# Kernel optimization log

Measured on AMD Instinct MI355X. Metric: run time of the kernel, lower is better.

The kernel has to match this reference:

```python
import jax, jax.numpy as jnp
import numpy as np

B, N, DIM, HEADS = 8, 4096, 512, 8
BASE = 10000.0


def rope_cos_sin(n, dim, base=BASE):
    k_max = dim // 2
    theta = 1.0 / base ** (jnp.arange(k_max, dtype=jnp.float32) / k_max)
    angles = jnp.arange(n, dtype=jnp.float32)[:, None] * theta  # (n, k_max)
    return jnp.cos(angles), jnp.sin(angles)


def apply_rope(x, cos, sin):
    # x: (b, n, dim); complex pairs are interleaved (even=real, odd=imag)
    xr = x[..., 0::2]
    xi = x[..., 1::2]
    out_r = cos * xr - sin * xi
    out_i = sin * xr + cos * xi
    return jnp.stack([out_r, out_i], axis=-1).reshape(x.shape)


def setup_inputs() -> dict:
    key = jax.random.key(0)
    ks = jax.random.split(key, 8)
    s = 0.02
    return {
        'x': jax.random.normal(ks[0], (B, N, DIM), jnp.float32),
        'y': jax.random.normal(ks[1], (B, N, DIM), jnp.float32),
        'Wq': jax.random.normal(ks[2], (DIM, DIM), jnp.float32) * s,
        'bq': jax.random.normal(ks[3], (DIM,), jnp.float32) * s,
        'Wk': jax.random.normal(ks[4], (DIM, DIM), jnp.float32) * s,
        'bk': jax.random.normal(ks[5], (DIM,), jnp.float32) * s,
        'lepe_w': jax.random.normal(ks[6], (DIM, 1, 3), jnp.float32) * s,
        'lepe_b': jax.random.normal(ks[7], (DIM,), jnp.float32) * s,
    }


def reference(x, y, Wq, bq, Wk, bk, lepe_w, lepe_b):
    b, n, c = x.shape
    h = HEADS
    d = c // h
    q = jax.nn.elu(x @ Wq.T + bq) + 1.0
    k = jax.nn.elu(y @ Wk.T + bk) + 1.0
    cos, sin = rope_cos_sin(n, c)
    q_rope = apply_rope(q, cos, sin).reshape(b, n, h, d).transpose(0, 2, 1, 3)
    k_rope = apply_rope(k, cos, sin).reshape(b, n, h, d).transpose(0, 2, 1, 3)
    qh = q.reshape(b, n, h, d).transpose(0, 2, 1, 3)
    kh = k.reshape(b, n, h, d).transpose(0, 2, 1, 3)
    v = y.reshape(b, n, h, d).transpose(0, 2, 1, 3)
    kmean = kh.mean(axis=2, keepdims=True)  # (b,h,1,d)
    z = 1.0 / (jnp.einsum('bhnd,bhmd->bhnm', qh, kmean) + 1e-6)  # (b,h,n,1)
    scale = n ** (-0.5)
    kv = jnp.einsum('bhnd,bhne->bhde', k_rope * scale, v * scale)  # (b,h,d,d)
    out = jnp.einsum('bhnd,bhde->bhne', q_rope, kv) * z  # (b,h,n,d)
    out = out.transpose(0, 2, 1, 3).reshape(b, n, c)
    # LePE: depthwise conv1d over value stream
    vc = v.transpose(0, 2, 1, 3).reshape(b, n, c).transpose(0, 2, 1)  # (b,c,n)
    lepe = jax.lax.conv_general_dilated(
        vc, lepe_w, window_strides=(1,), padding=[(1, 1)],
        dimension_numbers=('NCH', 'OIH', 'NCH'), feature_group_count=c)
    lepe = lepe + lepe_b[None, :, None]
    return out + lepe.transpose(0, 2, 1)
```

## Files before the change

kernel.cpp:

```cpp
#include <hip/hip_runtime.h>

#define B_ 8
#define N_ 4096
#define C_ 512
#define H_ 8

typedef _Float16 h8  __attribute__((ext_vector_type(8)));
typedef _Float16 h4v __attribute__((ext_vector_type(4)));
typedef float    f4  __attribute__((ext_vector_type(4)));

static const size_t OFF_COS  = 0;
static const size_t OFF_SIN  = (size_t)4*1024*1024;
static const size_t OFF_KRH  = (size_t)8*1024*1024;
static const size_t OFF_WQH  = (size_t)40*1024*1024;
static const size_t OFF_WKH  = (size_t)40*1024*1024 + 512*1024;
static const size_t OFF_KSUM = (size_t)41*1024*1024;
static const size_t OFF_KVG  = (size_t)41*1024*1024 + 64*1024;
static const size_t OFF_KVT  = (size_t)42*1024*1024 + 64*1024;

__device__ __forceinline__ unsigned int pack2h(float a, float b){
    union { _Float16 h[2]; unsigned int u; } x;
    x.h[0] = (_Float16)a; x.h[1] = (_Float16)b; return x.u;
}

__global__ void k_tables(float* __restrict__ cosT, float* __restrict__ sinT){
    int n = blockIdx.x, j = threadIdx.x;
    double th = exp((double)j * -0.035977892078031970);
    float ang = (float)n * (float)th;
    float s, c; sincosf(ang, &s, &c);
    cosT[n*256 + j] = c; sinT[n*256 + j] = s;
}

__global__ __launch_bounds__(256) void k_prepw(const float* __restrict__ Wq, const float* __restrict__ Wk,
                                               _Float16* __restrict__ Wqh, _Float16* __restrict__ Wkh){
    int u = blockIdx.x*256 + threadIdx.x;
    {
        float4 a = *(const float4*)&Wq[(size_t)u*8];
        float4 b = *(const float4*)&Wq[(size_t)u*8 + 4];
        uint4 o; o.x = pack2h(a.x,a.y); o.y = pack2h(a.z,a.w); o.z = pack2h(b.x,b.y); o.w = pack2h(b.z,b.w);
        *(uint4*)&Wqh[(size_t)u*8] = o;
    }
    {
        float4 a = *(const float4*)&Wk[(size_t)u*8];
        float4 b = *(const float4*)&Wk[(size_t)u*8 + 4];
        uint4 o; o.x = pack2h(a.x,a.y); o.y = pack2h(a.z,a.w); o.z = pack2h(b.x,b.y); o.w = pack2h(b.z,b.w);
        *(uint4*)&Wkh[(size_t)u*8] = o;
    }
}

__device__ __forceinline__ void stage_b(const _Float16* __restrict__ g, _Float16* lds, int t){
#pragma unroll
    for (int i=0;i<2;++i){
        int u = i*256 + t;
        int r = u >> 2;
        int c8 = (u & 3) ^ ((r ^ (r >> 2)) & 3);
        __builtin_amdgcn_global_load_lds(
            (const __attribute__((address_space(1))) void*)(g + (size_t)r*C_ + c8*8),
            (__attribute__((address_space(3))) void*)(lds + (size_t)(i*256 + (t & 192))*8),
            16, 0, 0);
    }
}

template<int IS_Q>
__global__ __launch_bounds__(256, 2) void k_gemm(
    const float* __restrict__ X, const _Float16* __restrict__ Wh, const float* __restrict__ bias,
    const float* __restrict__ cosT, const float* __restrict__ sinT,
    _Float16* __restrict__ krh, float* __restrict__ ksum,
    const float* __restrict__ ksumIn, const _Float16* __restrict__ kvTg,
    const float* __restrict__ y, const float* __restrict__ lw, const float* __restrict__ lb,
    float* __restrict__ outp)
{
    __shared__ __align__(16) char smem[IS_Q ? 55296 : 26624];
    _Float16* As  = (_Float16*)smem;
    _Float16* Bs0 = (_Float16*)(smem + 10240);
    _Float16* Bs1 = (_Float16*)(smem + 18432);
    _Float16* qrs = (_Float16*)smem;
    _Float16* kvs = (_Float16*)(smem + 36864);

    const int t = threadIdx.x;
    const int lane = t & 63;
    const int w = t >> 6;
    const int wm = w >> 1, wn = w & 1;
    const int col0 = blockIdx.x * 128;
    const int row0 = blockIdx.y * 128;
    const int lrow = lane & 15, lg = lane >> 4;
    const int srow = t >> 3;
    const int sc4 = (t & 7) * 4;
    const int b = row0 >> 12;

    if constexpr (IS_Q){
#pragma unroll
        for (int i=0;i<4;++i){
            int idx = i*256 + t;
            int hl = idx >> 9, e = (idx >> 3) & 63, c8 = idx & 7;
            int bhh = b*H_ + (col0 >> 6) + hl;
            *(uint4*)&kvs[hl*4608 + e*72 + c8*8] =
                *(const uint4*)&kvTg[(size_t)bhh*4096 + e*64 + c8*8];
        }
    }

    f4 acc[4][4] = {};
    const float* Xp = X + (size_t)(row0 + srow)*C_ + sc4;
    float4 ra[4];
#pragma unroll
    for (int it=0; it<4; ++it) ra[it] = *(const float4*)(Xp + (size_t)it*32*C_);
    stage_b(Wh + (size_t)col0*C_, Bs0, t);

    const int sw = (lrow ^ (lrow >> 2)) & 3;
    const int cB = (lg ^ sw) * 8;
    _Float16* Bcur = Bs0; _Float16* Bnxt = Bs1;

    for (int kk=0; kk<16; ++kk){
#pragma unroll
        for (int it=0; it<4; ++it){
            int r = srow + it*32;
            h4v a; a[0]=(_Float16)ra[it].x; a[1]=(_Float16)ra[it].y; a[2]=(_Float16)ra[it].z; a[3]=(_Float16)ra[it].w;
            *(h4v*)&As[r*40 + sc4] = a;
        }
        if (kk < 15){
#pragma unroll
            for (int it=0; it<4; ++it)
                ra[it] = *(const float4*)(Xp + (size_t)it*32*C_ + (kk+1)*32);
            stage_b(Wh + (size_t)col0*C_ + (kk+1)*32, Bnxt, t);
        }
        __syncthreads();
        h8 af[4], bf[4];
#pragma unroll
        for (int mi=0; mi<4; ++mi) af[mi] = *(const h8*)&As[(wm*64 + mi*16 + lrow)*40 + lg*8];
#pragma unroll
        for (int ni=0; ni<4; ++ni) bf[ni] = *(const h8*)&Bcur[(wn*64 + ni*16 + lrow)*32 + cB];
#pragma unroll
        for (int mi=0; mi<4; ++mi)
#pragma unroll
            for (int ni=0; ni<4; ++ni)
                acc[mi][ni] = __builtin_amdgcn_mfma_f32_16x16x32_f16(af[mi], bf[ni], acc[mi][ni], 0,0,0);
        __syncthreads();
        _Float16* tmp = Bcur; Bcur = Bnxt; Bnxt = tmp;
    }

    const int hcol0 = col0 + wn*64;
    float bcol[4], km[4];
#pragma unroll
    for (int ni=0; ni<4; ++ni){
        int c = hcol0 + ni*16 + lrow;
        bcol[ni] = bias[c];
        km[ni] = IS_Q ? ksumIn[b*C_ + c] * (1.0f/4096.0f) : 0.0f;
    }
    float colsum[4] = {0.f,0.f,0.f,0.f};
    float zr[4][4];
    _Float16* qw = qrs + w*4608;

#pragma unroll
    for (int mi=0; mi<4; ++mi){
        float qv[4][4];
#pragma unroll
        for (int ni=0; ni<4; ++ni)
#pragma unroll
            for (int r=0; r<4; ++r){
                float v = acc[mi][ni][r] + bcol[ni];
                qv[ni][r] = v > 0.f ? v + 1.f : __expf(v);
            }
        if constexpr (IS_Q){
#pragma unroll
            for (int r=0; r<4; ++r){
                float p = qv[0][r]*km[0] + qv[1][r]*km[1] + qv[2][r]*km[2] + qv[3][r]*km[3];
                p += __shfl_xor(p, 1); p += __shfl_xor(p, 2);
                p += __shfl_xor(p, 4); p += __shfl_xor(p, 8);
                zr[mi][r] = 1.0f / (p + 1e-6f);
            }
        } else {
#pragma unroll
            for (int ni=0; ni<4; ++ni)
                colsum[ni] += qv[ni][0]+qv[ni][1]+qv[ni][2]+qv[ni][3];
        }
#pragma unroll
        for (int ni=0; ni<4; ++ni){
            int c = hcol0 + ni*16 + lrow;
            int jj = c >> 1;
#pragma unroll
            for (int r=0; r<4; ++r){
                int grow = row0 + wm*64 + mi*16 + lg*4 + r;
                int n = grow & (N_-1);
                float val = qv[ni][r];
                float par = __shfl_xor(val, 1);
                float cs = cosT[n*256 + jj], sn = sinT[n*256 + jj];
                float rv = (lane & 1) ? fmaf(sn, par, cs*val) : fmaf(cs, val, -sn*par);
                float prv = __shfl_xor(rv, 1);
                if constexpr (IS_Q){
                    if (!(lane & 1))
                        *(unsigned int*)&qw[(mi*16 + lg*4 + r)*72 + (ni*16 + lrow)] = pack2h(rv, prv);
                } else {
                    if (!(lane & 1))
                        *(unsigned int*)&krh[(size_t)grow*C_ + c] = pack2h(rv, prv);
                }
            }
        }
    }

    if constexpr (!IS_Q){
#pragma unroll
        for (int ni=0; ni<4; ++ni){
            float s = colsum[ni];
            s += __shfl_xor(s, 16); s += __shfl_xor(s, 32);
            if (lane < 16) atomicAdd(&ksum[b*C_ + hcol0 + ni*16 + lane], s);
        }
    } else {
        f4 acc2[4][4] = {};
#pragma unroll
        for (int ks=0; ks<2; ++ks){
            h8 af2[4], bf2[4];
#pragma unroll
            for (int mi2=0; mi2<4; ++mi2) af2[mi2] = *(const h8*)&qw[(mi2*16 + lrow)*72 + ks*32 + lg*8];
#pragma unroll
            for (int ni2=0; ni2<4; ++ni2) bf2[ni2] = *(const h8*)&kvs[wn*4608 + (ni2*16 + lrow)*72 + ks*32 + lg*8];
#pragma unroll
            for (int mi2=0; mi2<4; ++mi2)
#pragma unroll
                for (int ni2=0; ni2<4; ++ni2)
                    acc2[mi2][ni2] = __builtin_amdgcn_mfma_f32_16x16x32_f16(af2[mi2], bf2[ni2], acc2[mi2][ni2], 0,0,0);
        }
        float w0[4], w1[4], w2[4], wb[4];
#pragma unroll
        for (int ni2=0; ni2<4; ++ni2){
            int cc = hcol0 + ni2*16 + lrow;
            w0[ni2]=lw[cc*3+0]; w1[ni2]=lw[cc*3+1]; w2[ni2]=lw[cc*3+2]; wb[ni2]=lb[cc];
        }
#pragma unroll
        for (int mi2=0; mi2<4; ++mi2){
#pragma unroll
            for (int r=0; r<4; ++r){
                int grow = row0 + wm*64 + mi2*16 + lg*4 + r;
                int n = grow & (N_-1);
                float z = zr[mi2][r];
#pragma unroll
                for (int ni2=0; ni2<4; ++ni2){
                    int c = hcol0 + ni2*16 + lrow;
                    const float* yp = y + (size_t)grow*C_ + c;
                    float s = fmaf(yp[0], w1[ni2], wb[ni2]);
                    if (n > 0)      s = fmaf(*(yp - C_), w0[ni2], s);
                    if (n < N_-1)   s = fmaf(*(yp + C_), w2[ni2], s);
                    outp[(size_t)grow*C_ + c] = fmaf(acc2[mi2][ni2][r], z, s);
                }
            }
        }
    }
}

__global__ __launch_bounds__(256) void k_kv(const _Float16* __restrict__ krh, const float* __restrict__ y,
                                            float* __restrict__ kvg){
    __shared__ _Float16 krs[64*128];
    __shared__ _Float16 vs[64*128];
    const int split = blockIdx.x, bh = blockIdx.y;
    const int b = bh >> 3, h = bh & 7;
    const int t = threadIdx.x, lane = t & 63, w = t >> 6;
    const int lrow = lane & 15, lg = lane >> 4;
    f4 acc[4] = {};
    for (int sub=0; sub<4; ++sub){
        const int n0 = split*512 + sub*128;
#pragma unroll
        for (int i=0;i<8;++i){
            int q = i*256 + t;
            int d2 = q & 31, n2 = q >> 5;
            int n = n0 + 2*n2, c = h*64 + 2*d2;
            size_t g0 = (size_t)(b*N_ + n)*C_ + c;
            unsigned int u0 = *(const unsigned int*)&krh[g0];
            unsigned int u1 = *(const unsigned int*)&krh[g0 + C_];
            int chunk = n2 >> 2, j2 = (n2 & 3)*2;
            int pc0 = chunk ^ ((2*d2) & 15);
            int pc1 = pc0 ^ 1;
            *(unsigned int*)&krs[(2*d2)*128 + pc0*8 + j2]   = (u0 & 0xffffu) | (u1 << 16);
            *(unsigned int*)&krs[(2*d2+1)*128 + pc1*8 + j2] = (u0 >> 16) | (u1 & 0xffff0000u);
            float2 a0 = *(const float2*)&y[g0];
            float2 a1 = *(const float2*)&y[g0 + C_];
            *(unsigned int*)&vs[(2*d2)*128 + pc0*8 + j2]   = pack2h(a0.x, a1.x);
            *(unsigned int*)&vs[(2*d2+1)*128 + pc1*8 + j2] = pack2h(a0.y, a1.y);
        }
        __syncthreads();
#pragma unroll
        for (int ks=0; ks<4; ++ks){
            int cu = ((ks*4 + lg) ^ lrow)*8;
            h8 a = *(const h8*)&krs[(w*16 + lrow)*128 + cu];
#pragma unroll
            for (int ni=0; ni<4; ++ni){
                h8 bv = *(const h8*)&vs[(ni*16 + lrow)*128 + cu];
                acc[ni] = __builtin_amdgcn_mfma_f32_16x16x32_f16(a, bv, acc[ni], 0,0,0);
            }
        }
        __syncthreads();
    }
#pragma unroll
    for (int ni=0; ni<4; ++ni)
#pragma unroll
        for (int rr=0; rr<4; ++rr)
            atomicAdd(&kvg[(size_t)bh*4096 + (w*16 + lg*4 + rr)*64 + ni*16 + lrow],
                      acc[ni][rr] * (1.0f/4096.0f));
}

__global__ __launch_bounds__(256) void k_kvmerge(const float* __restrict__ kvg, _Float16* __restrict__ kvTg){
    int bh = blockIdx.x, t = threadIdx.x;
    const float* src = kvg + (size_t)bh*4096;
    _Float16* dst = kvTg + (size_t)bh*4096;
#pragma unroll
    for (int i=0;i<4;++i){
        int q = i*256 + t;
        int e2 = q & 31, d2 = q >> 5;
        float2 a0 = *(const float2*)&src[(2*d2)*64 + 2*e2];
        float2 a1 = *(const float2*)&src[(2*d2+1)*64 + 2*e2];
        *(unsigned int*)&dst[(2*e2)*64 + 2*d2]   = pack2h(a0.x, a1.x);
        *(unsigned int*)&dst[(2*e2+1)*64 + 2*d2] = pack2h(a0.y, a1.y);
    }
}

extern "C" void kernel_launch(void* const* d_in, const int* in_sizes, int n_in,
                              void* d_out, int out_size, void* d_ws, size_t ws_size,
                              hipStream_t stream)
{
    (void)in_sizes; (void)n_in; (void)out_size; (void)ws_size;
    const float* x  = (const float*)d_in[0];
    const float* y  = (const float*)d_in[1];
    const float* Wq = (const float*)d_in[2];
    const float* bq = (const float*)d_in[3];
    const float* Wk = (const float*)d_in[4];
    const float* bk = (const float*)d_in[5];
    const float* lw = (const float*)d_in[6];
    const float* lb = (const float*)d_in[7];

    char* ws = (char*)d_ws;
    float*    cosT = (float*)(ws + OFF_COS);
    float*    sinT = (float*)(ws + OFF_SIN);
    _Float16* krh  = (_Float16*)(ws + OFF_KRH);
    _Float16* Wqh  = (_Float16*)(ws + OFF_WQH);
    _Float16* Wkh  = (_Float16*)(ws + OFF_WKH);
    float*    ksum = (float*)(ws + OFF_KSUM);
    float*    kvg  = (float*)(ws + OFF_KVG);
    _Float16* kvTg = (_Float16*)(ws + OFF_KVT);
    float*    out  = (float*)d_out;

    hipMemsetAsync(ws + OFF_KSUM, 0, 64*1024 + 1024*1024, stream);
    k_tables<<<dim3(N_), dim3(256), 0, stream>>>(cosT, sinT);
    k_prepw<<<dim3(128), dim3(256), 0, stream>>>(Wq, Wk, Wqh, Wkh);
    k_gemm<0><<<dim3(4, 256), dim3(256), 0, stream>>>(y, Wkh, bk, cosT, sinT,
        krh, ksum, nullptr, nullptr, nullptr, nullptr, nullptr, nullptr);
    k_kv<<<dim3(8, 64), dim3(256), 0, stream>>>(krh, y, kvg);
    k_kvmerge<<<dim3(64), dim3(256), 0, stream>>>(kvg, kvTg);
    k_gemm<1><<<dim3(4, 256), dim3(256), 0, stream>>>(x, Wqh, bq, cosT, sinT,
        nullptr, nullptr, ksum, kvTg, y, lw, lb, out);
}
```

Baseline: 199.5 us.

## Double-buffer A tile, raise occupancy, and vectorize LePE epilogue via LDS staging

```diff
diff --git a/kernel.cpp b/kernel.cpp
--- a/kernel.cpp
+++ b/kernel.cpp
@@ -62,7 +62,7 @@
 }
 
 template<int IS_Q>
-__global__ __launch_bounds__(256, 2) void k_gemm(
+__global__ __launch_bounds__(256, IS_Q ? 3 : 4) void k_gemm(
     const float* __restrict__ X, const _Float16* __restrict__ Wh, const float* __restrict__ bias,
     const float* __restrict__ cosT, const float* __restrict__ sinT,
     _Float16* __restrict__ krh, float* __restrict__ ksum,
@@ -70,10 +70,7 @@
     const float* __restrict__ y, const float* __restrict__ lw, const float* __restrict__ lb,
     float* __restrict__ outp)
 {
-    __shared__ __align__(16) char smem[IS_Q ? 55296 : 26624];
-    _Float16* As  = (_Float16*)smem;
-    _Float16* Bs0 = (_Float16*)(smem + 10240);
-    _Float16* Bs1 = (_Float16*)(smem + 18432);
+    __shared__ __align__(16) char smem[IS_Q ? 53248 : 36864];
     _Float16* qrs = (_Float16*)smem;
     _Float16* kvs = (_Float16*)(smem + 36864);
 
@@ -88,57 +85,59 @@
     const int sc4 = (t & 7) * 4;
     const int b = row0 >> 12;
 
-    if constexpr (IS_Q){
-#pragma unroll
-        for (int i=0;i<4;++i){
-            int idx = i*256 + t;
-            int hl = idx >> 9, e = (idx >> 3) & 63, c8 = idx & 7;
-            int bhh = b*H_ + (col0 >> 6) + hl;
-            *(uint4*)&kvs[hl*4608 + e*72 + c8*8] =
-                *(const uint4*)&kvTg[(size_t)bhh*4096 + e*64 + c8*8];
-        }
-    }
-
     f4 acc[4][4] = {};
     const float* Xp = X + (size_t)(row0 + srow)*C_ + sc4;
     float4 ra[4];
 #pragma unroll
     for (int it=0; it<4; ++it) ra[it] = *(const float4*)(Xp + (size_t)it*32*C_);
-    stage_b(Wh + (size_t)col0*C_, Bs0, t);
+    stage_b(Wh + (size_t)col0*C_, (_Float16*)(smem + 20480), t);
 
     const int sw = (lrow ^ (lrow >> 2)) & 3;
     const int cB = (lg ^ sw) * 8;
-    _Float16* Bcur = Bs0; _Float16* Bnxt = Bs1;
+    int cur = 0;
 
     for (int kk=0; kk<16; ++kk){
+        _Float16* As = (_Float16*)(smem + cur*10240);
 #pragma unroll
         for (int it=0; it<4; ++it){
             int r = srow + it*32;
             h4v a; a[0]=(_Float16)ra[it].x; a[1]=(_Float16)ra[it].y; a[2]=(_Float16)ra[it].z; a[3]=(_Float16)ra[it].w;
             *(h4v*)&As[r*40 + sc4] = a;
         }
+        __syncthreads();
         if (kk < 15){
 #pragma unroll
             for (int it=0; it<4; ++it)
                 ra[it] = *(const float4*)(Xp + (size_t)it*32*C_ + (kk+1)*32);
-            stage_b(Wh + (size_t)col0*C_ + (kk+1)*32, Bnxt, t);
-        }
-        __syncthreads();
+            stage_b(Wh + (size_t)col0*C_ + (kk+1)*32, (_Float16*)(smem + 20480 + (cur^1)*8192), t);
+        }
+        _Float16* Bs = (_Float16*)(smem + 20480 + cur*8192);
         h8 af[4], bf[4];
 #pragma unroll
         for (int mi=0; mi<4; ++mi) af[mi] = *(const h8*)&As[(wm*64 + mi*16 + lrow)*40 + lg*8];
 #pragma unroll
-        for (int ni=0; ni<4; ++ni) bf[ni] = *(const h8*)&Bcur[(wn*64 + ni*16 + lrow)*32 + cB];
+        for (int ni=0; ni<4; ++ni) bf[ni] = *(const h8*)&Bs[(wn*64 + ni*16 + lrow)*32 + cB];
 #pragma unroll
         for (int mi=0; mi<4; ++mi)
 #pragma unroll
             for (int ni=0; ni<4; ++ni)
                 acc[mi][ni] = __builtin_amdgcn_mfma_f32_16x16x32_f16(af[mi], bf[ni], acc[mi][ni], 0,0,0);
-        __syncthreads();
-        _Float16* tmp = Bcur; Bcur = Bnxt; Bnxt = tmp;
-    }
+        cur ^= 1;
+    }
+    __syncthreads();
 
     const int hcol0 = col0 + wn*64;
+    if constexpr (IS_Q){
+#pragma unroll
+        for (int i=0;i<4;++i){
+            int idx = i*256 + t;
+            int hl = idx >> 9, e = (idx >> 3) & 63, u = idx & 7;
+            int du = u ^ (e & 7);
+            int bhh = b*H_ + (col0 >> 6) + hl;
+            *(uint4*)&kvs[hl*4096 + e*64 + u*8] =
+                *(const uint4*)&kvTg[(size_t)bhh*4096 + e*64 + du*8];
+        }
+    }
     float bcol[4], km[4];
 #pragma unroll
     for (int ni=0; ni<4; ++ni){
@@ -205,6 +204,7 @@
             if (lane < 16) atomicAdd(&ksum[b*C_ + hcol0 + ni*16 + lane], s);
         }
     } else {
+        __syncthreads();
         f4 acc2[4][4] = {};
 #pragma unroll
         for (int ks=0; ks<2; ++ks){
@@ -212,36 +212,69 @@
 #pragma unroll
             for (int mi2=0; mi2<4; ++mi2) af2[mi2] = *(const h8*)&qw[(mi2*16 + lrow)*72 + ks*32 + lg*8];
 #pragma unroll
-            for (int ni2=0; ni2<4; ++ni2) bf2[ni2] = *(const h8*)&kvs[wn*4608 + (ni2*16 + lrow)*72 + ks*32 + lg*8];
+            for (int ni2=0; ni2<4; ++ni2){
+                int e = ni2*16 + lrow;
+                int du = ((ks*4 + lg) ^ (e & 7)) * 8;
+                bf2[ni2] = *(const h8*)&kvs[wn*4096 + e*64 + du];
+            }
 #pragma unroll
             for (int mi2=0; mi2<4; ++mi2)
 #pragma unroll
                 for (int ni2=0; ni2<4; ++ni2)
                     acc2[mi2][ni2] = __builtin_amdgcn_mfma_f32_16x16x32_f16(af2[mi2], bf2[ni2], acc2[mi2][ni2], 0,0,0);
         }
+#pragma unroll
+        for (int mi2=0; mi2<4; ++mi2){
+#pragma unroll
+            for (int r=0; r<4; ++r){
+                float z = zr[mi2][r];
+#pragma unroll
+                for (int ni2=0; ni2<4; ++ni2){
+                    float val = acc2[mi2][ni2][r] * z;
+                    float pv = __shfl_xor(val, 1);
+                    if (!(lane & 1))
+                        *(unsigned int*)&qw[(mi2*16 + lg*4 + r)*72 + (ni2*16 + lrow)] = pack2h(val, pv);
+                }
+            }
+        }
+        __syncthreads();
+        const int cg = t & 31;
+        const int c4p = cg * 4;
+        const int hl = c4p >> 6;
+        const int e0 = c4p & 63;
         float w0[4], w1[4], w2[4], wb[4];
 #pragma unroll
-        for (int ni2=0; ni2<4; ++ni2){
-            int cc = hcol0 + ni2*16 + lrow;
-            w0[ni2]=lw[cc*3+0]; w1[ni2]=lw[cc*3+1]; w2[ni2]=lw[cc*3+2]; wb[ni2]=lb[cc];
-        }
-#pragma unroll
-        for (int mi2=0; mi2<4; ++mi2){
-#pragma unroll
-            for (int r=0; r<4; ++r){
-                int grow = row0 + wm*64 + mi2*16 + lg*4 + r;
-                int n = grow & (N_-1);
-                float z = zr[mi2][r];
-#pragma unroll
-                for (int ni2=0; ni2<4; ++ni2){
-                    int c = hcol0 + ni2*16 + lrow;
-                    const float* yp = y + (size_t)grow*C_ + c;
-                    float s = fmaf(yp[0], w1[ni2], wb[ni2]);
-                    if (n > 0)      s = fmaf(*(yp - C_), w0[ni2], s);
-                    if (n < N_-1)   s = fmaf(*(yp + C_), w2[ni2], s);
-                    outp[(size_t)grow*C_ + c] = fmaf(acc2[mi2][ni2][r], z, s);
-                }
-            }
+        for (int j=0;j<4;++j){
+            int cc = col0 + c4p + j;
+            w0[j]=lw[cc*3+0]; w1[j]=lw[cc*3+1]; w2[j]=lw[cc*3+2]; wb[j]=lb[cc];
+        }
+#pragma unroll
+        for (int i=0;i<16;++i){
+            int rl = (t >> 5) + i*8;
+            int grow = row0 + rl;
+            int nloc = grow & (N_-1);
+            int wreg = (rl >> 6)*2 + hl;
+            h4v a = *(const h4v*)&qrs[wreg*4608 + (rl & 63)*72 + e0];
+            const float* yp = y + (size_t)grow*C_ + col0 + c4p;
+            float4 y1 = *(const float4*)yp;
+            float s0 = fmaf(y1.x, w1[0], wb[0]);
+            float s1 = fmaf(y1.y, w1[1], wb[1]);
+            float s2 = fmaf(y1.z, w1[2], wb[2]);
+            float s3 = fmaf(y1.w, w1[3], wb[3]);
+            if (nloc > 0){
+                float4 y0 = *(const float4*)(yp - C_);
+                s0 = fmaf(y0.x, w0[0], s0); s1 = fmaf(y0.y, w0[1], s1);
+                s2 = fmaf(y0.z, w0[2], s2); s3 = fmaf(y0.w, w0[3], s3);
+            }
+            if (nloc < N_-1){
+                float4 y2 = *(const float4*)(yp + C_);
+                s0 = fmaf(y2.x, w2[0], s0); s1 = fmaf(y2.y, w2[1], s1);
+                s2 = fmaf(y2.z, w2[2], s2); s3 = fmaf(y2.w, w2[3], s3);
+            }
+            float4 o;
+            o.x = (float)a[0] + s0; o.y = (float)a[1] + s1;
+            o.z = (float)a[2] + s2; o.w = (float)a[3] + s3;
+            *(float4*)&outp[(size_t)grow*C_ + col0 + c4p] = o;
         }
     }
 }
```

Measured after the change: 214.7 us. +7.6%, slower.
